# Kernel tuning notes

Measured on AMD Instinct MI355X. Metric: run time of the kernel, lower is better.

The kernel has to match this reference:

```python
import jax, jax.numpy as jnp
import numpy as np

B, T, F = 256, 2048, 20
H_NODES = 256


def _heaviside(x):
    # smooth heaviside approx used throughout the original module
    return (jnp.tanh(10.0 * x) + 1.0) * 0.5


def _evap(wu, wl, wd, pet):
    h = _heaviside
    et1 = h(wu - pet) * pet + h(pet - wu) * wu
    rp = h(pet - et1) * (pet - et1)  # h(-(pet-et1))*0 term vanishes
    et22 = h(rp - wl) * wl + h(wl - rp) * rp
    et2 = h(rp) * et22
    et33 = h(rp - et2 - wd) * wd + h(wd - (rp - et2)) * (rp - et2)
    et3 = h(rp - et2) * et33
    return et1, et2, et3


def _runoff(wu, wl, wd, p, wum, wlm, wdm, b, c):
    wum = wum * 19.9 + 0.1
    wlm = wlm * 30.0 + 60.0
    wdm = wdm * 60.0 + 60.0
    c = c * 0.19 + 0.01
    b = b * 0.3 + 0.1
    w_total = wum + wlm + wdm
    s = c * (wu / w_total) ** 2 + b * (wl / w_total) ** 2
    return _heaviside(p - s) * (p - s)


def _partition(runoff, k1, k2, k3):
    k1 = k1 * 0.69 + 0.01
    k2 = k2 * 0.69 + 0.01
    k3 = k3 * 0.89 + 0.01
    sr = k1 * runoff
    itf = k2 * (runoff - sr)
    bf = k3 * (runoff - sr - itf)
    return sr, itf, bf


def setup_inputs() -> dict:
    key = jax.random.key(0)
    ks = jax.random.split(key, 7)
    u = lambda k, shp: jax.random.uniform(k, shp, jnp.float32, -0.05, 0.05)
    inputs = jax.random.uniform(ks[0], (B, T, F), jnp.float32)
    return {
        "inputs": inputs,
        "w1": u(ks[1], (15, H_NODES)),
        "b1": jnp.zeros((H_NODES,), jnp.float32),
        "w2": u(ks[2], (H_NODES, 64)),
        "b2": jnp.zeros((64,), jnp.float32),
        "w3": u(ks[3], (64, 8)),
        "b3": jnp.zeros((8,), jnp.float32),
    }


def reference(inputs, w1, b1, w2, b2, w3, b3):
    pet = inputs[..., 0:1]
    tmean = inputs[..., 1:2]
    p = inputs[..., 2:3]
    attrs = inputs[..., 5:]  # [B,T,15]

    # static-attribute -> physical-parameter MLP
    h1 = jnp.tanh(attrs @ w1 + b1)
    h2 = jnp.tanh(h1 @ w2 + b2)
    params = jax.nn.sigmoid(h2 @ w3 + b3)  # [B,T,8]

    xs = jnp.concatenate([pet, p, tmean, params], axis=-1)  # [B,T,11]

    def step(state, x):
        wu, wl, wd = state[:, 0:1], state[:, 1:2], state[:, 2:3]
        pet_t, p_t = x[:, 0:1], x[:, 1:2]
        et1, et2, et3 = _evap(wu, wl, wd, pet_t)
        clip = lambda d: jnp.clip(d, -1e5, 1e5)
        wu_n = wu + clip(p_t - et1)
        wl_n = wl + clip(p_t - et1 - et2)
        wd_n = wd + clip(p_t - et1 - et2 - et3)
        ns = jnp.concatenate([wu_n, wl_n, wd_n], axis=1)  # [B,3]
        return ns, ns

    init = jnp.zeros((inputs.shape[0], 3), inputs.dtype)
    _, outs = jax.lax.scan(step, init, jnp.swapaxes(xs, 0, 1))  # [T,B,3]
    outputs = jnp.swapaxes(outs, 0, 1)  # [B,T,3]

    wu, wl, wd = outputs[..., 0:1], outputs[..., 1:2], outputs[..., 2:3]
    wum, wlm, wdm = params[..., 0:1], params[..., 1:2], params[..., 2:3]
    b, c = params[..., 3:4], params[..., 4:5]
    k1, k2, k3 = params[..., 5:6], params[..., 6:7], params[..., 7:8]

    et1, et2, et3 = _evap(wu, wl, wd, pet)
    # NOTE: original call() swaps (wl,wd) and (wlm,wdm) here - kept faithful
    runoff = _runoff(wu, wd, wl, p, wum, wdm, wlm, b, c)
    sr, itf, bf = _partition(runoff, k1, k2, k3)
    total_q = sr + itf * 0.5 + bf * 0.25  # flow routing
    return total_q  # [B,T,1]
```

## Files before the change

### kernel.cpp

```cpp
#include <hip/hip_runtime.h>

#define B_ 256
#define T_ 2048
#define F_ 20
#define NT (B_*T_)
#define CH 16
#define NCH (T_/CH)

typedef __bf16 bf16x8 __attribute__((ext_vector_type(8)));
typedef float  f32x4  __attribute__((ext_vector_type(4)));

__device__ __forceinline__ float ex2(float x){ return __builtin_amdgcn_exp2f(x); }
__device__ __forceinline__ float rcpf_(float x){ return __builtin_amdgcn_rcpf(x); }

#define K10F 28.853900817779268f
#define K1F   2.8853900817779268f
#define LOG2E 1.4426950408889634f

__device__ __forceinline__ float hside(float x){ return 1.0f - rcpf_(ex2(K10F*x) + 1.0f); }
__device__ __forceinline__ float tanh_f(float z){ return 1.0f - 2.0f*rcpf_(ex2(K1F*z) + 1.0f); }
__device__ __forceinline__ float sigmoid_f(float z){ return rcpf_(1.0f + ex2(-LOG2E*z)); }


__global__ __launch_bounds__(256) void prep_kernel(const float* __restrict__ in,
                                                   float* __restrict__ ws){
  int r = blockIdx.x*256 + threadIdx.x;
  if (r >= NT) return;
  int b = r & (B_-1);
  int t = r >> 8;
  const float* src = in + ((size_t)b*T_ + t)*F_;
  ((float2*)ws)[r] = make_float2(src[0], src[2]);
}

__global__ __launch_bounds__(512) void fused_kernel(const float* __restrict__ in,
    const float* __restrict__ w1, const float* __restrict__ b1,
    const float* __restrict__ w2, const float* __restrict__ b2,
    const float* __restrict__ w3, const float* __restrict__ b3,
    float* __restrict__ ws){
  extern __shared__ char sm[];
  float* pk4 = ws + 4*(size_t)NT;

  if (blockIdx.x < 4) {
    asm volatile("s_setprio 3");
    const float2* pp2 = (const float2*)ws;
    float* wuT = ws + 2*(size_t)NT;
    float* wdT = ws + 3*(size_t)NT;
    float*  d1L = (float*)sm;
    float*  bsQ = (float*)(sm + 8192);
    float2* rhL = (float2*)(sm + 24576);
    float2* qbL = (float2*)(sm + 40960);

    int tid = threadIdx.x;
    int wv = tid >> 6, lane = tid & 63;
    int boff = blockIdx.x * 64;

    float wu = 0.0f, wl = 0.0f, wd = 0.0f;
    float2 buf[2][8];

    if (wv == 0){
      #pragma unroll
      for (int g = 0; g < 2; ++g)
        #pragma unroll
        for (int i = 0; i < 8; ++i)
          buf[g][i] = pp2[(g*8 + i)*B_ + boff + lane];
    }

    for (int it = 0; it < NCH + 3; ++it){
      if (wv == 0){
        if (it < NCH){
          int c = it, par = c & 1;
          #pragma unroll
          for (int g = 0; g < 2; ++g){
            #pragma unroll
            for (int i = 0; i < 8; ++i){
              int s = g*8 + i;
              float pet = buf[g][i].x, p = buf[g][i].y;
              float d  = wu - pet;
              float r1 = rcpf_(ex2(K10F*d) + 1.0f);
              float d1 = -d*r1;
              float base = (p - pet) + d1;
              wu += base;
              wuT[(c*CH + s)*B_ + boff + lane] = wu;
              d1L[par*(CH*64) + s*64 + lane] = d1;
              bsQ[(c&3)*(CH*64) + s*64 + lane] = base;
            }
            int cn = (c + 1 < NCH) ? c + 1 : c;
            #pragma unroll
            for (int i = 0; i < 8; ++i)
              buf[g][i] = pp2[(cn*CH + g*8 + i)*B_ + boff + lane];
          }
        }
      } else if (wv == 1){
        if (it >= 1 && it <= NCH){
          int c = it - 1, par = c & 1;
          #pragma unroll
          for (int s = 0; s < CH; ++s){
            float d1 = d1L[par*(CH*64) + s*64 + lane];
            float r2 = rcpf_(ex2(K10F*d1) + 1.0f);
            float rp = fmaf(-d1, r2, d1);
            float hrp = 1.0f - rcpf_(ex2(K10F*rp) + 1.0f);
            rhL[par*(CH*64) + s*64 + lane] = make_float2(rp, hrp);
          }
        }
      } else if (wv == 2){
        if (it >= 2 && it <= NCH + 1){
          int c = it - 2, par = c & 1;
          #pragma unroll
          for (int s = 0; s < CH; ++s){
            float2 rh  = rhL[par*(CH*64) + s*64 + lane];
            float base = bsQ[(c&3)*(CH*64) + s*64 + lane];
            float d2   = rh.x - wl;
            float r    = rcpf_(ex2(K10F*d2) + 1.0f);
            float et22 = fmaf(d2, r, wl);
            float et2  = rh.y * et22;
            float b2   = base - et2;
            wl += b2;
            qbL[par*(CH*64) + s*64 + lane] = make_float2(rh.x - et2, b2);
          }
        }
      } else if (wv == 3){
        if (it >= 3){
          int c = it - 3, par = c & 1;
          #pragma unroll
          for (int s = 0; s < CH; ++s){
            float2 qb  = qbL[par*(CH*64) + s*64 + lane];
            float hqv  = 1.0f - rcpf_(ex2(K10F*qb.x) + 1.0f);
            float d3   = qb.x - wd;
            float r    = rcpf_(ex2(K10F*d3) + 1.0f);
            float et33 = fmaf(d3, r, wd);
            float et3  = hqv * et33;
            wd += qb.y - et3;
            wdT[(c*CH + s)*B_ + boff + lane] = wd;
          }
        }
      }
      __syncthreads();
    }
    return;
  }

  __bf16* w1f  = (__bf16*)sm;
  __bf16* w2f  = (__bf16*)(sm + 8192);
  float*  b1s  = (float*)(sm + 40960);
  float*  b2s  = (float*)(sm + 41984);
  float*  w3s  = (float*)(sm + 42240);
  float*  b3s  = (float*)(sm + 44288);
  __bf16* hbufA= (__bf16*)(sm + 44320);

  int tid = threadIdx.x;

  for (int s = tid; s < 16*32*8; s += 512) w1f[s] = (__bf16)0.0f;
  __syncthreads();
  for (int idx = tid; idx < 15*256; idx += 512){
    int k = idx >> 8, n = idx & 255;
    int ct = n >> 4;
    int l  = ((k>>3)*16) + (n & 15);
    int j  = k & 7;
    w1f[(ct*32 + l)*8 + j] = (__bf16)w1[idx];
  }
  for (int idx = tid; idx < 256*64; idx += 512){
    int k = idx >> 6, n = idx & 63;
    int kb = k >> 5;
    int lq = (k >> 3) & 3;
    int j  = k & 7;
    int ct = n >> 4;
    int l  = lq*16 + (n & 15);
    w2f[((kb*4 + ct)*64 + l)*8 + j] = (__bf16)w2[idx];
  }
  if (tid < 256) b1s[tid] = b1[tid];
  if (tid < 64)  b2s[tid] = b2[tid];
  if (tid < 512) w3s[tid] = w3[tid];
  if (tid < 8)   b3s[tid] = b3[tid];
  __syncthreads();

  int lane = tid & 63;
  int wv   = tid >> 6;
  int m    = lane & 15;
  int q    = lane >> 4;
  int r0   = (blockIdx.x - 4)*128 + wv*16;

  int rowA = r0 + m;
  int bA = rowA & (B_-1), tA = rowA >> 8;
  const float* ap = in + ((size_t)bA*T_ + tA)*F_ + 5;
  bf16x8 a1;
  #pragma unroll
  for (int j = 0; j < 8; ++j){
    int k = q*8 + j;
    float v = (k < 15) ? ap[k] : 0.0f;
    a1[j] = (__bf16)v;
  }

  __bf16* hb = hbufA + wv*1152;
  f32x4 zero4 = {0.0f, 0.0f, 0.0f, 0.0f};
  bf16x8 zero8;
  #pragma unroll
  for (int j = 0; j < 8; ++j) zero8[j] = (__bf16)0.0f;

  f32x4 acc2[4] = {zero4, zero4, zero4, zero4};

  #pragma unroll
  for (int p = 0; p < 4; ++p){
    #pragma unroll
    for (int c4 = 0; c4 < 4; ++c4){
      int ct = p*4 + c4;
      bf16x8 bw = zero8;
      if (lane < 32) bw = *(const bf16x8*)&w1f[(ct*32 + lane)*8];
      f32x4 c1 = __builtin_amdgcn_mfma_f32_16x16x32_bf16(a1, bw, zero4, 0, 0, 0);
      int f = c4*16 + m;
      float bb = b1s[p*64 + f];
      #pragma unroll
      for (int i = 0; i < 4; ++i){
        float h = tanh_f(c1[i] + bb);
        hb[(q*4 + i)*72 + f] = (__bf16)h;
      }
    }
    #pragma unroll
    for (int kb = 0; kb < 2; ++kb){
      bf16x8 a2 = *(const bf16x8*)&hb[m*72 + q*8 + kb*32];
      #pragma unroll
      for (int ct = 0; ct < 4; ++ct){
        bf16x8 bw2 = *(const bf16x8*)&w2f[(((p*2 + kb)*4 + ct)*64 + lane)*8];
        acc2[ct] = __builtin_amdgcn_mfma_f32_16x16x32_bf16(a2, bw2, acc2[ct], 0, 0, 0);
      }
    }
  }

  #pragma unroll
  for (int ct = 0; ct < 4; ++ct){
    int f = ct*16 + m;
    float bb = b2s[f];
    #pragma unroll
    for (int i = 0; i < 4; ++i){
      float h = tanh_f(acc2[ct][i] + bb);
      hb[(q*4 + i)*72 + f] = (__bf16)h;
    }
  }

  float z0 = b3s[2*q], z1 = b3s[2*q + 1];
  #pragma unroll
  for (int kb3 = 0; kb3 < 8; ++kb3){
    bf16x8 hv8 = *(const bf16x8*)&hb[m*72 + kb3*8];
    #pragma unroll
    for (int j = 0; j < 8; ++j){
      float hv = (float)hv8[j];
      int k = kb3*8 + j;
      z0 = fmaf(hv, w3s[k*8 + 2*q],     z0);
      z1 = fmaf(hv, w3s[k*8 + 2*q + 1], z1);
    }
  }

  float* hf = (float*)hb;
  hf[m*8 + 2*q]     = sigmoid_f(z0);
  hf[m*8 + 2*q + 1] = sigmoid_f(z1);
  if (q == 0){
    float P0=hf[m*8+0], P1=hf[m*8+1], P2=hf[m*8+2], P3=hf[m*8+3];
    float P4=hf[m*8+4], P5=hf[m*8+5], P6=hf[m*8+6], P7=hf[m*8+7];
    float wum = fmaf(P0, 19.9f, 0.1f);
    float wlm = fmaf(P2, 30.0f, 60.0f);
    float wdm = fmaf(P1, 60.0f, 60.0f);
    float wt  = wum + wlm + wdm;
    float rw  = 1.0f / wt;
    float cc  = fmaf(P4, 0.19f, 0.01f);
    float bc  = fmaf(P3, 0.30f, 0.10f);
    float A   = cc*rw*rw;
    float Bc  = bc*rw*rw;
    float k1  = fmaf(P5, 0.69f, 0.01f);
    float k2  = fmaf(P6, 0.69f, 0.01f);
    float k3  = fmaf(P7, 0.89f, 0.01f);
    float KP  = k1 + 0.5f*k2*(1.0f-k1) + 0.25f*k3*(1.0f-k1)*(1.0f-k2);
    int rowO = r0 + m;
    *(float4*)&pk4[(size_t)rowO*4] = make_float4(A, Bc, KP, 0.0f);
  }
}

__global__ __launch_bounds__(256) void final_kernel(const float* __restrict__ ws,
                                                    float* __restrict__ out){
  __shared__ float tile[64*65];
  int tb = blockIdx.x & 31;
  int bb = blockIdx.x >> 5;
  int t0 = tb*64, b0 = bb*64;
  int tid = threadIdx.x;
  const float2* pp2 = (const float2*)ws;
  const float* wuT  = ws + 2*(size_t)NT;
  const float* wdT  = ws + 3*(size_t)NT;
  const float* pk4  = ws + 4*(size_t)NT;

  #pragma unroll
  for (int k = 0; k < 16; ++k){
    int idx = k*256 + tid;
    int tl = idx >> 6, bl = idx & 63;
    int r = (t0 + tl)*B_ + b0 + bl;
    float p  = pp2[r].y;
    float wu = wuT[r], wd = wdT[r];
    float4 k4 = *(const float4*)&pk4[(size_t)r*4];
    float ps = p - k4.x*wu*wu - k4.y*wd*wd;
    float runoff = hside(ps)*ps;
    tile[bl*65 + tl] = k4.z * runoff;
  }
  __syncthreads();
  #pragma unroll
  for (int k = 0; k < 16; ++k){
    int idx = k*256 + tid;
    int tl2 = idx & 63, bl2 = idx >> 6;
    out[(size_t)(b0 + bl2)*T_ + t0 + tl2] = tile[bl2*65 + tl2];
  }
}

extern "C" void kernel_launch(void* const* d_in, const int* in_sizes, int n_in,
                              void* d_out, int out_size, void* d_ws, size_t ws_size,
                              hipStream_t stream) {
  const float* in = (const float*)d_in[0];
  const float* w1 = (const float*)d_in[1];
  const float* b1 = (const float*)d_in[2];
  const float* w2 = (const float*)d_in[3];
  const float* b2 = (const float*)d_in[4];
  const float* w3 = (const float*)d_in[5];
  const float* b3 = (const float*)d_in[6];
  float* out = (float*)d_out;
  float* ws  = (float*)d_ws;

  prep_kernel <<<NT/256,     256, 0,     stream>>>(in, ws);
  fused_kernel<<<NT/128 + 4, 512, 62752, stream>>>(in, w1, b1, w2, b2, w3, b3, ws);
  final_kernel<<<128,        256, 0,     stream>>>(ws, out);
}
```

Baseline: 218.6 us.

## Split into MLP and flag-synchronized scan kernels with fused runoff output

Folds the pet/p extraction into the MLP kernel and moves the sequential moisture scan into its own 4-block kernel. Inside the scan, the block-wide barrier per chunk is replaced by per-wave LDS progress flags using acquire/release atomics, so the four pipeline waves advance independently. The last scan wave now computes runoff and routed flow directly and writes the output, which removes the separate final kernel and the wu/wd workspace round-trip. The cost is that the scan no longer overlaps the MLP work, and the last wave adds global loads per chunk to the serial critical path.

```diff
diff --git a/kernel.cpp b/kernel.cpp
--- a/kernel.cpp
+++ b/kernel.cpp
@@ -22,132 +22,28 @@
 __device__ __forceinline__ float sigmoid_f(float z){ return rcpf_(1.0f + ex2(-LOG2E*z)); }
 
 
-__global__ __launch_bounds__(256) void prep_kernel(const float* __restrict__ in,
-                                                   float* __restrict__ ws){
-  int r = blockIdx.x*256 + threadIdx.x;
-  if (r >= NT) return;
-  int b = r & (B_-1);
-  int t = r >> 8;
-  const float* src = in + ((size_t)b*T_ + t)*F_;
-  ((float2*)ws)[r] = make_float2(src[0], src[2]);
-}
-
-__global__ __launch_bounds__(512) void fused_kernel(const float* __restrict__ in,
+__global__ __launch_bounds__(512) void mlp_kernel(const float* __restrict__ in,
     const float* __restrict__ w1, const float* __restrict__ b1,
     const float* __restrict__ w2, const float* __restrict__ b2,
     const float* __restrict__ w3, const float* __restrict__ b3,
     float* __restrict__ ws){
-  extern __shared__ char sm[];
-  float* pk4 = ws + 4*(size_t)NT;
-
-  if (blockIdx.x < 4) {
-    asm volatile("s_setprio 3");
-    const float2* pp2 = (const float2*)ws;
-    float* wuT = ws + 2*(size_t)NT;
-    float* wdT = ws + 3*(size_t)NT;
-    float*  d1L = (float*)sm;
-    float*  bsQ = (float*)(sm + 8192);
-    float2* rhL = (float2*)(sm + 24576);
-    float2* qbL = (float2*)(sm + 40960);
-
-    int tid = threadIdx.x;
-    int wv = tid >> 6, lane = tid & 63;
-    int boff = blockIdx.x * 64;
-
-    float wu = 0.0f, wl = 0.0f, wd = 0.0f;
-    float2 buf[2][8];
-
-    if (wv == 0){
-      #pragma unroll
-      for (int g = 0; g < 2; ++g)
-        #pragma unroll
-        for (int i = 0; i < 8; ++i)
-          buf[g][i] = pp2[(g*8 + i)*B_ + boff + lane];
-    }
-
-    for (int it = 0; it < NCH + 3; ++it){
-      if (wv == 0){
-        if (it < NCH){
-          int c = it, par = c & 1;
-          #pragma unroll
-          for (int g = 0; g < 2; ++g){
-            #pragma unroll
-            for (int i = 0; i < 8; ++i){
-              int s = g*8 + i;
-              float pet = buf[g][i].x, p = buf[g][i].y;
-              float d  = wu - pet;
-              float r1 = rcpf_(ex2(K10F*d) + 1.0f);
-              float d1 = -d*r1;
-              float base = (p - pet) + d1;
-              wu += base;
-              wuT[(c*CH + s)*B_ + boff + lane] = wu;
-              d1L[par*(CH*64) + s*64 + lane] = d1;
-              bsQ[(c&3)*(CH*64) + s*64 + lane] = base;
-            }
-            int cn = (c + 1 < NCH) ? c + 1 : c;
-            #pragma unroll
-            for (int i = 0; i < 8; ++i)
-              buf[g][i] = pp2[(cn*CH + g*8 + i)*B_ + boff + lane];
-          }
-        }
-      } else if (wv == 1){
-        if (it >= 1 && it <= NCH){
-          int c = it - 1, par = c & 1;
-          #pragma unroll
-          for (int s = 0; s < CH; ++s){
-            float d1 = d1L[par*(CH*64) + s*64 + lane];
-            float r2 = rcpf_(ex2(K10F*d1) + 1.0f);
-            float rp = fmaf(-d1, r2, d1);
-            float hrp = 1.0f - rcpf_(ex2(K10F*rp) + 1.0f);
-            rhL[par*(CH*64) + s*64 + lane] = make_float2(rp, hrp);
-          }
-        }
-      } else if (wv == 2){
-        if (it >= 2 && it <= NCH + 1){
-          int c = it - 2, par = c & 1;
-          #pragma unroll
-          for (int s = 0; s < CH; ++s){
-            float2 rh  = rhL[par*(CH*64) + s*64 + lane];
-            float base = bsQ[(c&3)*(CH*64) + s*64 + lane];
-            float d2   = rh.x - wl;
-            float r    = rcpf_(ex2(K10F*d2) + 1.0f);
-            float et22 = fmaf(d2, r, wl);
-            float et2  = rh.y * et22;
-            float b2   = base - et2;
-            wl += b2;
-            qbL[par*(CH*64) + s*64 + lane] = make_float2(rh.x - et2, b2);
-          }
-        }
-      } else if (wv == 3){
-        if (it >= 3){
-          int c = it - 3, par = c & 1;
-          #pragma unroll
-          for (int s = 0; s < CH; ++s){
-            float2 qb  = qbL[par*(CH*64) + s*64 + lane];
-            float hqv  = 1.0f - rcpf_(ex2(K10F*qb.x) + 1.0f);
-            float d3   = qb.x - wd;
-            float r    = rcpf_(ex2(K10F*d3) + 1.0f);
-            float et33 = fmaf(d3, r, wd);
-            float et3  = hqv * et33;
-            wd += qb.y - et3;
-            wdT[(c*CH + s)*B_ + boff + lane] = wd;
-          }
-        }
-      }
-      __syncthreads();
-    }
-    return;
-  }
-
-  __bf16* w1f  = (__bf16*)sm;
-  __bf16* w2f  = (__bf16*)(sm + 8192);
-  float*  b1s  = (float*)(sm + 40960);
-  float*  b2s  = (float*)(sm + 41984);
-  float*  w3s  = (float*)(sm + 42240);
-  float*  b3s  = (float*)(sm + 44288);
-  __bf16* hbufA= (__bf16*)(sm + 44320);
-
+  __shared__ __bf16 w1f[16*32*8];
+  __shared__ __bf16 w2f[32*64*8];
+  __shared__ float  b1s[256];
+  __shared__ float  b2s[64];
+  __shared__ float  w3s[512];
+  __shared__ float  b3s[8];
+  __shared__ __bf16 hbufA[8*1152];
+
+  float* pk4 = ws + 2*(size_t)NT;
   int tid = threadIdx.x;
+
+  if (tid < 128){
+    int r = blockIdx.x*128 + tid;
+    int b = r & (B_-1), t = r >> 8;
+    const float* src = in + ((size_t)b*T_ + t)*F_;
+    ((float2*)ws)[r] = make_float2(src[0], src[2]);
+  }
 
   for (int s = tid; s < 16*32*8; s += 512) w1f[s] = (__bf16)0.0f;
   __syncthreads();
@@ -177,7 +73,7 @@
   int wv   = tid >> 6;
   int m    = lane & 15;
   int q    = lane >> 4;
-  int r0   = (blockIdx.x - 4)*128 + wv*16;
+  int r0   = blockIdx.x*128 + wv*16;
 
   int rowA = r0 + m;
   int bA = rowA & (B_-1), tA = rowA >> 8;
@@ -273,36 +169,165 @@
   }
 }
 
-__global__ __launch_bounds__(256) void final_kernel(const float* __restrict__ ws,
-                                                    float* __restrict__ out){
-  __shared__ float tile[64*65];
-  int tb = blockIdx.x & 31;
-  int bb = blockIdx.x >> 5;
-  int t0 = tb*64, b0 = bb*64;
-  int tid = threadIdx.x;
+struct ScanB {
+  float  d1L[2][CH][64];
+  float  bsQ[4][CH][64];
+  float2 rhL[2][CH][64];
+  float2 qbL[2][CH][64];
+  int    done[4*16];
+};
+
+__global__ __launch_bounds__(256) void scan_kernel(const float* __restrict__ ws,
+                                                   float* __restrict__ out){
+  __shared__ ScanB S;
   const float2* pp2 = (const float2*)ws;
-  const float* wuT  = ws + 2*(size_t)NT;
-  const float* wdT  = ws + 3*(size_t)NT;
-  const float* pk4  = ws + 4*(size_t)NT;
-
-  #pragma unroll
-  for (int k = 0; k < 16; ++k){
-    int idx = k*256 + tid;
-    int tl = idx >> 6, bl = idx & 63;
-    int r = (t0 + tl)*B_ + b0 + bl;
-    float p  = pp2[r].y;
-    float wu = wuT[r], wd = wdT[r];
-    float4 k4 = *(const float4*)&pk4[(size_t)r*4];
-    float ps = p - k4.x*wu*wu - k4.y*wd*wd;
-    float runoff = hside(ps)*ps;
-    tile[bl*65 + tl] = k4.z * runoff;
-  }
+  const float*  pk4 = ws + 2*(size_t)NT;
+
+  int tid  = threadIdx.x;
+  int wv   = tid >> 6;
+  int lane = tid & 63;
+  int boff = blockIdx.x * 64;
+  int bmy  = boff + lane;
+
+  if (tid < 64) S.done[tid] = 0;
   __syncthreads();
-  #pragma unroll
-  for (int k = 0; k < 16; ++k){
-    int idx = k*256 + tid;
-    int tl2 = idx & 63, bl2 = idx >> 6;
-    out[(size_t)(b0 + bl2)*T_ + t0 + tl2] = tile[bl2*65 + tl2];
+
+  auto publish = [&](int i, int v){
+    if (lane == 0)
+      __hip_atomic_store(&S.done[i*16], v, __ATOMIC_RELEASE, __HIP_MEMORY_SCOPE_WORKGROUP);
+  };
+  auto waitge = [&](int i, int v){
+    while (__hip_atomic_load(&S.done[i*16], __ATOMIC_ACQUIRE, __HIP_MEMORY_SCOPE_WORKGROUP) < v)
+      __builtin_amdgcn_s_sleep(1);
+  };
+
+  if (wv == 0){
+    float wu = 0.0f;
+    float2 bufA[CH], bufB[CH];
+    #pragma unroll
+    for (int s = 0; s < CH; ++s) bufA[s] = pp2[s*B_ + bmy];
+    #pragma unroll
+    for (int s = 0; s < CH; ++s) bufB[s] = pp2[(CH + s)*B_ + bmy];
+
+    for (int c = 0; c < NCH; c += 2){
+      waitge(1, c-1);
+      waitge(3, c-3);
+      #pragma unroll
+      for (int s = 0; s < CH; ++s){
+        float pet = bufA[s].x, p = bufA[s].y;
+        float d  = wu - pet;
+        float r1 = rcpf_(ex2(K10F*d) + 1.0f);
+        float d1 = -d*r1;
+        float base = (p - pet) + d1;
+        wu += base;
+        S.d1L[c&1][s][lane] = d1;
+        S.bsQ[c&3][s][lane] = base;
+      }
+      publish(0, c+1);
+      if (c + 2 < NCH){
+        #pragma unroll
+        for (int s = 0; s < CH; ++s) bufA[s] = pp2[((c+2)*CH + s)*B_ + bmy];
+      }
+      int c1 = c + 1;
+      waitge(1, c1-1);
+      waitge(3, c1-3);
+      #pragma unroll
+      for (int s = 0; s < CH; ++s){
+        float pet = bufB[s].x, p = bufB[s].y;
+        float d  = wu - pet;
+        float r1 = rcpf_(ex2(K10F*d) + 1.0f);
+        float d1 = -d*r1;
+        float base = (p - pet) + d1;
+        wu += base;
+        S.d1L[c1&1][s][lane] = d1;
+        S.bsQ[c1&3][s][lane] = base;
+      }
+      publish(0, c1+1);
+      if (c1 + 2 < NCH){
+        #pragma unroll
+        for (int s = 0; s < CH; ++s) bufB[s] = pp2[((c1+2)*CH + s)*B_ + bmy];
+      }
+    }
+  } else if (wv == 1){
+    for (int c = 0; c < NCH; ++c){
+      waitge(0, c+1);
+      waitge(2, c-1);
+      float d1_[CH];
+      #pragma unroll
+      for (int s = 0; s < CH; ++s) d1_[s] = S.d1L[c&1][s][lane];
+      float2 rh_[CH];
+      #pragma unroll
+      for (int s = 0; s < CH; ++s){
+        float r2 = rcpf_(ex2(K10F*d1_[s]) + 1.0f);
+        float rp = fmaf(-d1_[s], r2, d1_[s]);
+        float hrp = 1.0f - rcpf_(ex2(K10F*rp) + 1.0f);
+        rh_[s] = make_float2(rp, hrp);
+      }
+      #pragma unroll
+      for (int s = 0; s < CH; ++s) S.rhL[c&1][s][lane] = rh_[s];
+      publish(1, c+1);
+    }
+  } else if (wv == 2){
+    float wl = 0.0f;
+    for (int c = 0; c < NCH; ++c){
+      waitge(1, c+1);
+      waitge(3, c-1);
+      float2 rh_[CH]; float bs_[CH];
+      #pragma unroll
+      for (int s = 0; s < CH; ++s) rh_[s] = S.rhL[c&1][s][lane];
+      #pragma unroll
+      for (int s = 0; s < CH; ++s) bs_[s] = S.bsQ[c&3][s][lane];
+      float2 qb_[CH];
+      #pragma unroll
+      for (int s = 0; s < CH; ++s){
+        float d2   = rh_[s].x - wl;
+        float r    = rcpf_(ex2(K10F*d2) + 1.0f);
+        float et22 = fmaf(d2, r, wl);
+        float et2  = rh_[s].y * et22;
+        float b2   = bs_[s] - et2;
+        wl += b2;
+        qb_[s] = make_float2(rh_[s].x - et2, b2);
+      }
+      #pragma unroll
+      for (int s = 0; s < CH; ++s) S.qbL[c&1][s][lane] = qb_[s];
+      publish(2, c+1);
+    }
+  } else {
+    float wd = 0.0f, wu3 = 0.0f;
+    for (int c = 0; c < NCH; ++c){
+      waitge(2, c+1);
+      float4 k4_[CH]; float pv_[CH];
+      #pragma unroll
+      for (int s = 0; s < CH; ++s){
+        int r = (c*CH + s)*B_ + bmy;
+        k4_[s] = *(const float4*)&pk4[(size_t)r*4];
+        pv_[s] = pp2[r].y;
+      }
+      float2 qb_[CH]; float bs_[CH];
+      #pragma unroll
+      for (int s = 0; s < CH; ++s) qb_[s] = S.qbL[c&1][s][lane];
+      #pragma unroll
+      for (int s = 0; s < CH; ++s) bs_[s] = S.bsQ[c&3][s][lane];
+      float qv_[CH];
+      #pragma unroll
+      for (int s = 0; s < CH; ++s){
+        float hqv  = 1.0f - rcpf_(ex2(K10F*qb_[s].x) + 1.0f);
+        float d3   = qb_[s].x - wd;
+        float r    = rcpf_(ex2(K10F*d3) + 1.0f);
+        float et33 = fmaf(d3, r, wd);
+        float et3  = hqv * et33;
+        wd += qb_[s].y - et3;
+        wu3 += bs_[s];
+        float ps = pv_[s] - k4_[s].x*wu3*wu3 - k4_[s].y*wd*wd;
+        float runoff = hside(ps)*ps;
+        qv_[s] = k4_[s].z * runoff;
+      }
+      publish(3, c+1);
+      float* dst = out + (size_t)bmy*T_ + c*CH;
+      #pragma unroll
+      for (int g = 0; g < 4; ++g)
+        *(float4*)(dst + g*4) = make_float4(qv_[g*4], qv_[g*4+1], qv_[g*4+2], qv_[g*4+3]);
+    }
   }
 }
 
@@ -319,7 +344,6 @@
   float* out = (float*)d_out;
   float* ws  = (float*)d_ws;
 
-  prep_kernel <<<NT/256,     256, 0,     stream>>>(in, ws);
-  fused_kernel<<<NT/128 + 4, 512, 62752, stream>>>(in, w1, b1, w2, b2, w3, b3, ws);
-  final_kernel<<<128,        256, 0,     stream>>>(ws, out);
+  mlp_kernel <<<NT/128, 512, 0, stream>>>(in, w1, b1, w2, b2, w3, b3, ws);
+  scan_kernel<<<4,      256, 0, stream>>>(ws, out);
 }
```

After: 376.3 us. 1.72x slower.

## Rescale recurrence states by the heaviside constant and restructure the per-wave scan loops

Applied to the files above, without the earlier changes.

The scan state variables are now kept pre-multiplied by the tanh scale factor, which removes the multiply in front of each exp2 on the serial dependency chain. Updates are rewritten as fmas, and outputs are scaled back with a constant multiply. Each wave now runs its own loop with its own barrier calls, and wave 0 prefetches the whole next chunk before computing the current one. The prep kernel is also rewritten so each thread does more work, with float4 loads and fewer blocks. This trades extra registers and small rounding differences for a shorter critical path in the recurrence.

```diff
diff --git a/kernel.cpp b/kernel.cpp
--- a/kernel.cpp
+++ b/kernel.cpp
@@ -14,6 +14,7 @@
 __device__ __forceinline__ float rcpf_(float x){ return __builtin_amdgcn_rcpf(x); }
 
 #define K10F 28.853900817779268f
+#define INVK 0.034657359027997264f
 #define K1F   2.8853900817779268f
 #define LOG2E 1.4426950408889634f
 
@@ -24,12 +25,20 @@
 
 __global__ __launch_bounds__(256) void prep_kernel(const float* __restrict__ in,
                                                    float* __restrict__ ws){
-  int r = blockIdx.x*256 + threadIdx.x;
-  if (r >= NT) return;
-  int b = r & (B_-1);
-  int t = r >> 8;
-  const float* src = in + ((size_t)b*T_ + t)*F_;
-  ((float2*)ws)[r] = make_float2(src[0], src[2]);
+  int bt = blockIdx.x & 15;
+  int tt = blockIdx.x >> 4;
+  int b0 = bt*16, t0 = tt*128;
+  int bl = threadIdx.x & 15;
+  int tw = threadIdx.x >> 4;
+  int b  = b0 + bl;
+  const float* rowb = in + (size_t)b*T_*F_;
+  float2* pp2 = (float2*)ws;
+  #pragma unroll
+  for (int k = 0; k < 8; ++k){
+    int t = t0 + k*16 + tw;
+    float4 r4 = *(const float4*)(rowb + (size_t)t*F_);
+    pp2[t*B_ + b] = make_float2(r4.x, r4.z);
+  }
 }
 
 __global__ __launch_bounds__(512) void fused_kernel(const float* __restrict__ in,
@@ -54,89 +63,101 @@
     int wv = tid >> 6, lane = tid & 63;
     int boff = blockIdx.x * 64;
 
-    float wu = 0.0f, wl = 0.0f, wd = 0.0f;
-    float2 buf[2][8];
-
     if (wv == 0){
+      float2 buf[CH], nbuf[CH];
       #pragma unroll
-      for (int g = 0; g < 2; ++g)
-        #pragma unroll
-        for (int i = 0; i < 8; ++i)
-          buf[g][i] = pp2[(g*8 + i)*B_ + boff + lane];
-    }
-
-    for (int it = 0; it < NCH + 3; ++it){
-      if (wv == 0){
+      for (int s = 0; s < CH; ++s) buf[s] = pp2[s*B_ + boff + lane];
+      float Wu = 0.0f;
+      for (int it = 0; it < NCH + 3; ++it){
         if (it < NCH){
           int c = it, par = c & 1;
+          if (c + 1 < NCH){
+            #pragma unroll
+            for (int s = 0; s < CH; ++s) nbuf[s] = pp2[((c+1)*CH + s)*B_ + boff + lane];
+          }
           #pragma unroll
-          for (int g = 0; g < 2; ++g){
+          for (int s = 0; s < CH; ++s){
+            float PET = K10F*buf[s].x;
+            float PPd = K10F*(buf[s].y - buf[s].x);
+            float t1  = Wu - PET;
+            float r   = rcpf_(ex2(t1) + 1.0f);
+            float dK  = -t1*r;
+            float BS  = PPd + dK;
+            float WuPP= Wu + PPd;
+            Wu = fmaf(-t1, r, WuPP);
+            d1L[par*(CH*64) + s*64 + lane] = dK;
+            bsQ[(c&3)*(CH*64) + s*64 + lane] = BS;
+            wuT[(c*CH + s)*B_ + boff + lane] = Wu * INVK;
+          }
+          if (c + 1 < NCH){
             #pragma unroll
-            for (int i = 0; i < 8; ++i){
-              int s = g*8 + i;
-              float pet = buf[g][i].x, p = buf[g][i].y;
-              float d  = wu - pet;
-              float r1 = rcpf_(ex2(K10F*d) + 1.0f);
-              float d1 = -d*r1;
-              float base = (p - pet) + d1;
-              wu += base;
-              wuT[(c*CH + s)*B_ + boff + lane] = wu;
-              d1L[par*(CH*64) + s*64 + lane] = d1;
-              bsQ[(c&3)*(CH*64) + s*64 + lane] = base;
-            }
-            int cn = (c + 1 < NCH) ? c + 1 : c;
-            #pragma unroll
-            for (int i = 0; i < 8; ++i)
-              buf[g][i] = pp2[(cn*CH + g*8 + i)*B_ + boff + lane];
+            for (int s = 0; s < CH; ++s) buf[s] = nbuf[s];
           }
         }
-      } else if (wv == 1){
+        __syncthreads();
+      }
+      return;
+    } else if (wv == 1){
+      for (int it = 0; it < NCH + 3; ++it){
         if (it >= 1 && it <= NCH){
           int c = it - 1, par = c & 1;
           #pragma unroll
           for (int s = 0; s < CH; ++s){
-            float d1 = d1L[par*(CH*64) + s*64 + lane];
-            float r2 = rcpf_(ex2(K10F*d1) + 1.0f);
-            float rp = fmaf(-d1, r2, d1);
-            float hrp = 1.0f - rcpf_(ex2(K10F*rp) + 1.0f);
-            rhL[par*(CH*64) + s*64 + lane] = make_float2(rp, hrp);
+            float dK = d1L[par*(CH*64) + s*64 + lane];
+            float r2 = rcpf_(ex2(dK) + 1.0f);
+            float RP = fmaf(-dK, r2, dK);
+            float HRP = 1.0f - rcpf_(ex2(RP) + 1.0f);
+            rhL[par*(CH*64) + s*64 + lane] = make_float2(RP, HRP);
           }
         }
-      } else if (wv == 2){
+        __syncthreads();
+      }
+      return;
+    } else if (wv == 2){
+      float WL = 0.0f;
+      for (int it = 0; it < NCH + 3; ++it){
         if (it >= 2 && it <= NCH + 1){
           int c = it - 2, par = c & 1;
           #pragma unroll
           for (int s = 0; s < CH; ++s){
             float2 rh  = rhL[par*(CH*64) + s*64 + lane];
-            float base = bsQ[(c&3)*(CH*64) + s*64 + lane];
-            float d2   = rh.x - wl;
-            float r    = rcpf_(ex2(K10F*d2) + 1.0f);
-            float et22 = fmaf(d2, r, wl);
-            float et2  = rh.y * et22;
-            float b2   = base - et2;
-            wl += b2;
-            qbL[par*(CH*64) + s*64 + lane] = make_float2(rh.x - et2, b2);
+            float BS   = bsQ[(c&3)*(CH*64) + s*64 + lane];
+            float D2   = rh.x - WL;
+            float r    = rcpf_(ex2(D2) + 1.0f);
+            float et22 = fmaf(D2, r, WL);
+            float ET2  = rh.y * et22;
+            float WLB  = WL + BS;
+            WL = fmaf(-rh.y, et22, WLB);
+            qbL[par*(CH*64) + s*64 + lane] = make_float2(rh.x - ET2, BS - ET2);
           }
         }
-      } else if (wv == 3){
+        __syncthreads();
+      }
+      return;
+    } else if (wv == 3){
+      float WD = 0.0f;
+      for (int it = 0; it < NCH + 3; ++it){
         if (it >= 3){
           int c = it - 3, par = c & 1;
           #pragma unroll
           for (int s = 0; s < CH; ++s){
             float2 qb  = qbL[par*(CH*64) + s*64 + lane];
-            float hqv  = 1.0f - rcpf_(ex2(K10F*qb.x) + 1.0f);
-            float d3   = qb.x - wd;
-            float r    = rcpf_(ex2(K10F*d3) + 1.0f);
-            float et33 = fmaf(d3, r, wd);
-            float et3  = hqv * et33;
-            wd += qb.y - et3;
-            wdT[(c*CH + s)*B_ + boff + lane] = wd;
+            float HQ   = 1.0f - rcpf_(ex2(qb.x) + 1.0f);
+            float D3   = qb.x - WD;
+            float r    = rcpf_(ex2(D3) + 1.0f);
+            float et33 = fmaf(D3, r, WD);
+            float WDB  = WD + qb.y;
+            WD = fmaf(-HQ, et33, WDB);
+            wdT[(c*CH + s)*B_ + boff + lane] = WD * INVK;
           }
         }
-      }
-      __syncthreads();
-    }
-    return;
+        __syncthreads();
+      }
+      return;
+    } else {
+      for (int it = 0; it < NCH + 3; ++it) __syncthreads();
+      return;
+    }
   }
 
   __bf16* w1f  = (__bf16*)sm;
@@ -319,7 +340,7 @@
   float* out = (float*)d_out;
   float* ws  = (float*)d_ws;
 
-  prep_kernel <<<NT/256,     256, 0,     stream>>>(in, ws);
+  prep_kernel <<<256,        256, 0,     stream>>>(in, ws);
   fused_kernel<<<NT/128 + 4, 512, 62752, stream>>>(in, w1, b1, w2, b2, w3, b3, ws);
   final_kernel<<<128,        256, 0,     stream>>>(ws, out);
 }
```

After: 224.4 us. 1.03x slower.
